# Kernel tuning notes

Hardware: AMD Instinct MI355X
Metric: run time of the kernel (lower is better)

Reference implementation:

```python
import jax, jax.numpy as jnp
import numpy as np

N = 10000       # nodes
E = 640000      # edges
D_IN = 128
D_OUT = 128
EPS = 1e-5      # LayerNorm eps (torch default)


def setup_inputs() -> dict:
    key = jax.random.key(0)
    k_x, k_e, k_w, k_b, k_g = jax.random.split(key, 5)
    x = jax.random.normal(k_x, (N, D_IN), dtype=jnp.float32)
    edge_index = jax.random.randint(k_e, (2, E), 0, N, dtype=jnp.int64)
    # GCNConv linear weight (PyG uses glorot) and bias
    lim = float(np.sqrt(6.0 / (D_IN + D_OUT)))
    W = jax.random.uniform(k_w, (D_IN, D_OUT), minval=-lim, maxval=lim, dtype=jnp.float32)
    b = jnp.zeros((D_OUT,), dtype=jnp.float32)
    # LayerNorm affine params
    gamma = jnp.ones((D_OUT,), dtype=jnp.float32)
    beta = jnp.zeros((D_OUT,), dtype=jnp.float32)
    return {"x": x, "edge_index": edge_index, "W": W, "b": b, "gamma": gamma, "beta": beta}


def reference(x, edge_index, W, b, gamma, beta):
    # --- GCNConv: A_hat = D^{-1/2} (A + I) D^{-1/2}; out = A_hat X W + b ---
    self_idx = jnp.arange(N, dtype=edge_index.dtype)
    src = jnp.concatenate([edge_index[0], self_idx])  # [E+N]
    dst = jnp.concatenate([edge_index[1], self_idx])  # [E+N]
    deg = jax.ops.segment_sum(jnp.ones_like(src, dtype=x.dtype), dst, num_segments=N)
    dinv = jnp.where(deg > 0, jax.lax.rsqrt(deg), 0.0)  # [N]
    norm = dinv[src] * dinv[dst]                        # [E+N]
    h = x @ W                                           # [N, D_OUT] transform first (cheaper)
    msg = h[src] * norm[:, None]                        # [E+N, D_OUT]
    out = jax.ops.segment_sum(msg, dst, num_segments=N) + b
    # --- LayerNorm over feature dim ---
    mu = jnp.mean(out, axis=-1, keepdims=True)
    var = jnp.mean(jnp.square(out - mu), axis=-1, keepdims=True)
    out = (out - mu) * jax.lax.rsqrt(var + EPS) * gamma + beta
    # act = Identity (last_act=ReLU is truthy -> Identity branch); dropout = eval identity; residual=False
    return out
```

## Files before the change

kernel.cpp:

```cpp
#include <hip/hip_runtime.h>
#include <hip/hip_fp16.h>

#define D 128
#define LN_EPS 1e-5f


static __device__ __forceinline__ float h2f(unsigned short h) {
    return __half2float(__builtin_bit_cast(__half, h));
}
static __device__ __forceinline__ unsigned short f2h(float f) {
    return __builtin_bit_cast(unsigned short, __float2half_rn(f));
}

__global__ __launch_bounds__(1024) void hist_kernel(const int* __restrict__ dst,
                                                    int* __restrict__ ghist,
                                                    const float* __restrict__ x,
                                                    unsigned int* __restrict__ xh,
                                                    const float* __restrict__ W,
                                                    unsigned int* __restrict__ Wh,
                                                    int N, int E, int Ec, int NH, int NW,
                                                    int C) {
    extern __shared__ int hist[];
    int c = blockIdx.x;
    bool is_hist = (c < C);
    if (is_hist)
        for (int i = threadIdx.x; i < N; i += blockDim.x) hist[i] = 0;
    int gs = gridDim.x * blockDim.x;
    int tot = NH + NW;
    for (int i = blockIdx.x * blockDim.x + threadIdx.x; i < tot; i += gs) {
        if (i < NH) {
            float2 v = ((const float2*)x)[i];
            xh[i] = (unsigned int)f2h(v.x) | ((unsigned int)f2h(v.y) << 16);
        } else {
            float2 v = ((const float2*)W)[i - NH];
            Wh[i - NH] = (unsigned int)f2h(v.x) | ((unsigned int)f2h(v.y) << 16);
        }
    }
    if (!is_hist) return;
    __syncthreads();
    int lo = c * Ec, hi = min(lo + Ec, E);
    for (int i = lo + threadIdx.x; i < hi; i += blockDim.x)
        atomicAdd(&hist[dst[i]], 1);
    __syncthreads();
    for (int i = threadIdx.x; i < N; i += blockDim.x) ghist[c * N + i] = hist[i];
}

__global__ void chunkoff_kernel(int* __restrict__ ghist, int* __restrict__ deg,
                                int N, int C) {
    int n = blockIdx.x * blockDim.x + threadIdx.x;
    if (n < N) {
        int run = 0;
        #pragma unroll 4
        for (int c = 0; c < C; c++) {
            int t = ghist[c * N + n];
            ghist[c * N + n] = run;
            run += t;
        }
        deg[n] = run;
    }
}

__global__ __launch_bounds__(1024) void scan_kernel(const int* __restrict__ deg,
                                                    int* __restrict__ rowptr,
                                                    int* __restrict__ fill,
                                                    float* __restrict__ dinv, int N) {
    __shared__ int s_wsum[16];
    __shared__ int s_woff[16];
    __shared__ int s_carry;
    int t = threadIdx.x;
    int lane = t & 63, w = t >> 6;
    if (t == 0) s_carry = 0;
    __syncthreads();
    for (int base = 0; base < N; base += 1024) {
        int i = base + t;
        int v = (i < N) ? deg[i] : 0;
        int incl = v;
        #pragma unroll
        for (int off = 1; off < 64; off <<= 1) {
            int y = __shfl_up(incl, off);
            if (lane >= off) incl += y;
        }
        if (lane == 63) s_wsum[w] = incl;
        __syncthreads();
        if (t == 0) {
            int run = s_carry;
            #pragma unroll
            for (int k = 0; k < 16; k++) { s_woff[k] = run; run += s_wsum[k]; }
            s_carry = run;
        }
        __syncthreads();
        if (i < N) {
            int rp = s_woff[w] + (incl - v);
            rowptr[i] = rp;
            fill[i] = rp;
            dinv[i] = rsqrtf((float)(v + 1));
        }
    }
    if (t == 0) rowptr[N] = s_carry;
}

__global__ __launch_bounds__(1024) void scatter_kernel(const int* __restrict__ src,
                                                       const int* __restrict__ dst,
                                                       const int* __restrict__ rowptr,
                                                       const int* __restrict__ goff,
                                                       unsigned short* __restrict__ csr,
                                                       int N, int E, int Ec) {
    extern __shared__ int cnt[];
    int c = blockIdx.x;
    for (int i = threadIdx.x; i < N; i += blockDim.x)
        cnt[i] = rowptr[i] + goff[c * N + i];
    __syncthreads();
    int lo = c * Ec, hi = min(lo + Ec, E);
    for (int i = lo + threadIdx.x; i < hi; i += blockDim.x) {
        int d = dst[i];
        int pos = atomicAdd(&cnt[d], 1);
        csr[pos] = (unsigned short)src[i];
    }
}

__global__ __launch_bounds__(512) void fused_fp16(const unsigned int* __restrict__ xh,
                                                  const unsigned int* __restrict__ Wh,
                                                  const int* __restrict__ rowptr,
                                                  const unsigned short* __restrict__ csr,
                                                  const float* __restrict__ dinv,
                                                  const float* __restrict__ bias,
                                                  const float* __restrict__ gamma,
                                                  const float* __restrict__ beta,
                                                  float* __restrict__ out, int N) {
    int w = threadIdx.x >> 6, lane = threadIdx.x & 63;
    int node = blockIdx.x * 8 + w;
    if (node >= N) return;
    float dn = dinv[node];

    unsigned int xv = xh[node * 64 + lane];
    float a0 = h2f((unsigned short)xv) * dn * dn;
    float a1 = h2f((unsigned short)(xv >> 16)) * dn * dn;

    int start = rowptr[node], end = rowptr[node + 1];
    int base = start;
    for (; base + 64 <= end; base += 64) {
        int s = csr[base + lane];
        float wt = dinv[s] * dn;
        #pragma unroll 8
        for (int k = 0; k < 64; k++) {
            int sk = __shfl(s, k);
            float wk = __shfl(wt, k);
            unsigned int hv = xh[sk * 64 + lane];
            a0 += h2f((unsigned short)hv) * wk;
            a1 += h2f((unsigned short)(hv >> 16)) * wk;
        }
    }
    int rem = end - base;
    if (rem > 0) {
        int s = 0; float wt = 0.f;
        if (lane < rem) { s = csr[base + lane]; wt = dinv[s] * dn; }
        for (int k = 0; k < rem; k++) {
            int sk = __shfl(s, k);
            float wk = __shfl(wt, k);
            unsigned int hv = xh[sk * 64 + lane];
            a0 += h2f((unsigned short)hv) * wk;
            a1 += h2f((unsigned short)(hv >> 16)) * wk;
        }
    }

    int c0 = lane * 2;
    float y0 = bias[c0], y1 = bias[c0 + 1];
    #pragma unroll 8
    for (int k = 0; k < 64; k++) {
        float g0 = __shfl(a0, k);
        float g1 = __shfl(a1, k);
        unsigned int w0 = Wh[(2 * k) * 64 + lane];
        unsigned int w1 = Wh[(2 * k + 1) * 64 + lane];
        y0 += g0 * h2f((unsigned short)w0) + g1 * h2f((unsigned short)w1);
        y1 += g0 * h2f((unsigned short)(w0 >> 16)) + g1 * h2f((unsigned short)(w1 >> 16));
    }

    float sum = y0 + y1, sq = y0 * y0 + y1 * y1;
    #pragma unroll
    for (int off = 32; off > 0; off >>= 1) {
        sum += __shfl_xor(sum, off);
        sq  += __shfl_xor(sq, off);
    }
    float mean = sum * (1.0f / D);
    float var  = sq * (1.0f / D) - mean * mean;
    float inv  = rsqrtf(var + LN_EPS);
    float o0 = (y0 - mean) * inv * gamma[c0] + beta[c0];
    float o1 = (y1 - mean) * inv * gamma[c0 + 1] + beta[c0 + 1];
    *(float2*)(out + (size_t)node * D + c0) = make_float2(o0, o1);
}


__global__ void deg_kernel(const int* __restrict__ dst, int* __restrict__ deg, int E) {
    int e = blockIdx.x * blockDim.x + threadIdx.x;
    if (e < E) atomicAdd(&deg[dst[e]], 1);
}
__global__ void fill_kernel(const int* __restrict__ src, const int* __restrict__ dst,
                            int* __restrict__ fill, unsigned short* __restrict__ csr, int E) {
    int e = blockIdx.x * blockDim.x + threadIdx.x;
    if (e < E) {
        int pos = atomicAdd(&fill[dst[e]], 1);
        csr[pos] = (unsigned short)src[e];
    }
}
__global__ __launch_bounds__(512) void fused_fp32(const float* __restrict__ x,
                                                  const float* __restrict__ W,
                                                  const int* __restrict__ rowptr,
                                                  const unsigned short* __restrict__ csr,
                                                  const float* __restrict__ dinv,
                                                  const float* __restrict__ bias,
                                                  const float* __restrict__ gamma,
                                                  const float* __restrict__ beta,
                                                  float* __restrict__ out, int N) {
    __shared__ float sW[D * D];
    {
        const float4* Wv = (const float4*)W;
        float4* sWv = (float4*)sW;
        #pragma unroll
        for (int i = 0; i < (D * D / 4) / 512; i++)
            sWv[threadIdx.x + i * 512] = Wv[threadIdx.x + i * 512];
    }
    __syncthreads();
    int w = threadIdx.x >> 6, lane = threadIdx.x & 63;
    int node = blockIdx.x * 8 + w;
    if (node >= N) return;
    float dn = dinv[node];
    int c0 = lane * 2;
    float2 xv = *(const float2*)(x + (size_t)node * D + c0);
    float a0 = xv.x * dn * dn, a1 = xv.y * dn * dn;
    int start = rowptr[node], end = rowptr[node + 1];
    int base = start;
    for (; base + 64 <= end; base += 64) {
        int s = csr[base + lane];
        float wt = dinv[s] * dn;
        #pragma unroll 8
        for (int k = 0; k < 64; k++) {
            int sk = __shfl(s, k);
            float wk = __shfl(wt, k);
            float2 xs = *(const float2*)(x + (size_t)sk * D + c0);
            a0 += xs.x * wk; a1 += xs.y * wk;
        }
    }
    int rem = end - base;
    if (rem > 0) {
        int s = 0; float wt = 0.f;
        if (lane < rem) { s = csr[base + lane]; wt = dinv[s] * dn; }
        for (int k = 0; k < rem; k++) {
            int sk = __shfl(s, k);
            float wk = __shfl(wt, k);
            float2 xs = *(const float2*)(x + (size_t)sk * D + c0);
            a0 += xs.x * wk; a1 += xs.y * wk;
        }
    }
    float y0 = bias[c0], y1 = bias[c0 + 1];
    #pragma unroll 8
    for (int k = 0; k < 64; k++) {
        float g0 = __shfl(a0, k);
        float g1 = __shfl(a1, k);
        float2 w0 = *(const float2*)(sW + (2 * k) * D + c0);
        float2 w1 = *(const float2*)(sW + (2 * k + 1) * D + c0);
        y0 += g0 * w0.x + g1 * w1.x;
        y1 += g0 * w0.y + g1 * w1.y;
    }
    float sum = y0 + y1, sq = y0 * y0 + y1 * y1;
    #pragma unroll
    for (int off = 32; off > 0; off >>= 1) {
        sum += __shfl_xor(sum, off);
        sq  += __shfl_xor(sq, off);
    }
    float mean = sum * (1.0f / D);
    float var  = sq * (1.0f / D) - mean * mean;
    float inv  = rsqrtf(var + LN_EPS);
    float o0 = (y0 - mean) * inv * gamma[c0] + beta[c0];
    float o1 = (y1 - mean) * inv * gamma[c0 + 1] + beta[c0 + 1];
    *(float2*)(out + (size_t)node * D + c0) = make_float2(o0, o1);
}

extern "C" void kernel_launch(void* const* d_in, const int* in_sizes, int n_in,
                              void* d_out, int out_size, void* d_ws, size_t ws_size,
                              hipStream_t stream) {
    const float* x     = (const float*)d_in[0];
    const int*   ei    = (const int*)d_in[1];
    const float* W     = (const float*)d_in[2];
    const float* bias  = (const float*)d_in[3];
    const float* gamma = (const float*)d_in[4];
    const float* beta  = (const float*)d_in[5];
    float*       out   = (float*)d_out;

    int N = in_sizes[0] / D;
    int E = in_sizes[1] / 2;
    const int* src = ei;
    const int* dst = ei + E;

    char* ws = (char*)d_ws;
    size_t off = 0;
    auto carve = [&](size_t bytes) { size_t p = off; off = (off + bytes + 15) & ~15UL; return (void*)(ws + p); };
    int*            deg    = (int*)           carve((size_t)N * 4);
    int*            rowptr = (int*)           carve((size_t)(N + 1) * 4);
    int*            fill   = (int*)           carve((size_t)N * 4);
    float*          dinv   = (float*)         carve((size_t)N * 4);
    unsigned short* csr    = (unsigned short*)carve((size_t)E * 2);
    unsigned short* xhbuf  = (unsigned short*)carve((size_t)N * D * 2);
    unsigned int*   Wh     = (unsigned int*)  carve((size_t)D * D / 2 * 4);
    size_t fixed_end = off;

    int C = 0;
    if (ws_size > fixed_end + 16) {
        size_t avail = ws_size - fixed_end - 16;
        size_t cmax = avail / ((size_t)N * 4);
        C = (int)((cmax > 64) ? 64 : cmax);
    }

    if (C >= 8) {
        int* ghist = (int*)carve((size_t)C * N * 4);
        unsigned int* xh = (unsigned int*)xhbuf;
        int Ec = (E + C - 1) / C;
        int NH = N * (D / 2);
        int NW = D * D / 2;
        size_t lds = (size_t)N * 4;
        int hist_grid = (256 > C) ? 256 : C;
        hist_kernel<<<hist_grid, 1024, lds, stream>>>(dst, ghist, x, xh, W, Wh,
                                                      N, E, Ec, NH, NW, C);
        chunkoff_kernel<<<(N + 255) / 256, 256, 0, stream>>>(ghist, deg, N, C);
        scan_kernel<<<1, 1024, 0, stream>>>(deg, rowptr, fill, dinv, N);
        scatter_kernel<<<C, 1024, lds, stream>>>(src, dst, rowptr, ghist, csr, N, E, Ec);
        fused_fp16<<<(N + 7) / 8, 512, 0, stream>>>(xh, Wh, rowptr, csr, dinv, bias, gamma, beta, out, N);
    } else {
        hipMemsetAsync(deg, 0, (size_t)N * 4, stream);
        deg_kernel<<<(E + 255) / 256, 256, 0, stream>>>(dst, deg, E);
        scan_kernel<<<1, 1024, 0, stream>>>(deg, rowptr, fill, dinv, N);
        fill_kernel<<<(E + 255) / 256, 256, 0, stream>>>(src, dst, fill, csr, E);
        fused_fp32<<<(N + 7) / 8, 512, 0, stream>>>(x, W, rowptr, csr, dinv, bias, gamma, beta, out, N);
    }
}
```

Measured before the change: 154.4 us.

## Merge CSR build stages into one persistent kernel with grid barriers

Replaces the hist, chunk-offset, single-block scan and scatter kernels with one build kernel of C blocks that synchronise through atomic grid barriers. It also parallelises the prefix scan across blocks with a two-level blocksum scan. The aggregation kernel now has two waves share each node, splitting the edge list, and combines the results in LDS before an LDS-based matvec and LayerNorm. The aim is to cut kernel launch gaps and the serial scan. The risks are that the fp16 conversion now runs on only C blocks, and that the spin barriers rely on all C blocks being co-resident.

```diff
diff --git a/kernel.cpp b/kernel.cpp
--- a/kernel.cpp
+++ b/kernel.cpp
@@ -12,22 +12,34 @@
     return __builtin_bit_cast(unsigned short, __float2half_rn(f));
 }
 
-__global__ __launch_bounds__(1024) void hist_kernel(const int* __restrict__ dst,
-                                                    int* __restrict__ ghist,
-                                                    const float* __restrict__ x,
-                                                    unsigned int* __restrict__ xh,
-                                                    const float* __restrict__ W,
-                                                    unsigned int* __restrict__ Wh,
-                                                    int N, int E, int Ec, int NH, int NW,
-                                                    int C) {
-    extern __shared__ int hist[];
+static __device__ __forceinline__ void gbar(int* cnt, int target) {
+    __syncthreads();
+    if (threadIdx.x == 0) {
+        __hip_atomic_fetch_add(cnt, 1, __ATOMIC_RELEASE, __HIP_MEMORY_SCOPE_AGENT);
+        while (__hip_atomic_load(cnt, __ATOMIC_ACQUIRE, __HIP_MEMORY_SCOPE_AGENT) < target) {
+            __builtin_amdgcn_s_sleep(1);
+        }
+    }
+    __syncthreads();
+}
+
+__global__ __launch_bounds__(1024) void build_kernel(
+        const int* __restrict__ src, const int* __restrict__ dst,
+        const float* __restrict__ x, const float* __restrict__ W,
+        unsigned int* __restrict__ xh, unsigned int* __restrict__ Wh,
+        int* __restrict__ ghist, int* __restrict__ blocksum,
+        int* __restrict__ rowptr, float* __restrict__ dinv,
+        unsigned short* __restrict__ csr, int* __restrict__ bar,
+        int N, int E, int Ec, int NH, int NW, int C) {
+    extern __shared__ int lds[];
     int c = blockIdx.x;
-    bool is_hist = (c < C);
-    if (is_hist)
-        for (int i = threadIdx.x; i < N; i += blockDim.x) hist[i] = 0;
-    int gs = gridDim.x * blockDim.x;
+    int tid = threadIdx.x;
+    int lane = tid & 63, wv = tid >> 6;
+
+    for (int i = tid; i < N; i += 1024) lds[i] = 0;
+    int gs = gridDim.x * 1024;
     int tot = NH + NW;
-    for (int i = blockIdx.x * blockDim.x + threadIdx.x; i < tot; i += gs) {
+    for (int i = c * 1024 + tid; i < tot; i += gs) {
         if (i < NH) {
             float2 v = ((const float2*)x)[i];
             xh[i] = (unsigned int)f2h(v.x) | ((unsigned int)f2h(v.y) << 16);
@@ -36,30 +48,162 @@
             Wh[i - NH] = (unsigned int)f2h(v.x) | ((unsigned int)f2h(v.y) << 16);
         }
     }
-    if (!is_hist) return;
     __syncthreads();
     int lo = c * Ec, hi = min(lo + Ec, E);
-    for (int i = lo + threadIdx.x; i < hi; i += blockDim.x)
-        atomicAdd(&hist[dst[i]], 1);
-    __syncthreads();
-    for (int i = threadIdx.x; i < N; i += blockDim.x) ghist[c * N + i] = hist[i];
-}
-
-__global__ void chunkoff_kernel(int* __restrict__ ghist, int* __restrict__ deg,
-                                int N, int C) {
-    int n = blockIdx.x * blockDim.x + threadIdx.x;
-    if (n < N) {
+    for (int i = lo + tid; i < hi; i += 1024)
+        atomicAdd(&lds[dst[i]], 1);
+    __syncthreads();
+    for (int i = tid; i < N; i += 1024) ghist[c * N + i] = lds[i];
+    gbar(bar + 0, C);
+
+    int nper = (N + C - 1) / C;
+    int n0 = c * nper;
+    int nn = min(nper, N - n0); if (nn < 0) nn = 0;
+    int mydeg = 0;
+    if (tid < nn) {
+        int n = n0 + tid;
         int run = 0;
-        #pragma unroll 4
-        for (int c = 0; c < C; c++) {
-            int t = ghist[c * N + n];
-            ghist[c * N + n] = run;
+        #pragma unroll 8
+        for (int cc = 0; cc < C; cc++) {
+            int t = ghist[cc * N + n];
+            ghist[cc * N + n] = run;
             run += t;
         }
-        deg[n] = run;
-    }
-}
-
+        mydeg = run;
+        dinv[n] = rsqrtf((float)(run + 1));
+    }
+    int incl = mydeg;
+    #pragma unroll
+    for (int off = 1; off < 64; off <<= 1) {
+        int y = __shfl_up(incl, off);
+        if (lane >= off) incl += y;
+    }
+    __syncthreads();
+    if (lane == 63) lds[wv] = incl;
+    __syncthreads();
+    if (tid == 0) {
+        int run = 0;
+        #pragma unroll
+        for (int k = 0; k < 16; k++) { int t = lds[k]; lds[k] = run; run += t; }
+        lds[16] = run;
+    }
+    __syncthreads();
+    int excl = lds[wv] + incl - mydeg;
+    if (tid < nn) rowptr[n0 + tid] = excl;
+    if (tid == 0) blocksum[c] = lds[16];
+    gbar(bar + 1, C);
+
+    __syncthreads();
+    if (wv == 0) {
+        int bs = (lane < C) ? blocksum[lane] : 0;
+        int inc2 = bs;
+        #pragma unroll
+        for (int off = 1; off < 64; off <<= 1) {
+            int y = __shfl_up(inc2, off);
+            if (lane >= off) inc2 += y;
+        }
+        if (lane == C - 1) lds[17] = inc2;
+        if (lane == c)     lds[18] = inc2 - bs;
+    }
+    __syncthreads();
+    int base = lds[18];
+    if (tid < nn) rowptr[n0 + tid] += base;
+    if (c == C - 1 && tid == 0) rowptr[N] = lds[17];
+    gbar(bar + 2, C);
+
+    for (int i = tid; i < N; i += 1024) lds[i] = rowptr[i] + ghist[c * N + i];
+    __syncthreads();
+    for (int i = lo + tid; i < hi; i += 1024) {
+        int d = dst[i];
+        int pos = atomicAdd(&lds[d], 1);
+        csr[pos] = (unsigned short)src[i];
+    }
+}
+
+__global__ __launch_bounds__(512) void fused2(const unsigned int* __restrict__ xh,
+                                              const unsigned int* __restrict__ Wh,
+                                              const int* __restrict__ rowptr,
+                                              const unsigned short* __restrict__ csr,
+                                              const float* __restrict__ dinv,
+                                              const float* __restrict__ bias,
+                                              const float* __restrict__ gamma,
+                                              const float* __restrict__ beta,
+                                              float* __restrict__ out, int N) {
+    __shared__ float sAgg[4][D];
+    __shared__ float sRed[4][2][2];
+    int wv = threadIdx.x >> 6, lane = threadIdx.x & 63;
+    int pair = wv >> 1, half = wv & 1;
+    int node = blockIdx.x * 4 + pair;
+    bool valid = (node < N);
+    int node_c = valid ? node : (N - 1);
+    float dn = dinv[node_c];
+
+    float a0 = 0.f, a1 = 0.f;
+    if (half == 0) {
+        unsigned int xv = xh[node_c * 64 + lane];
+        a0 = h2f((unsigned short)xv) * dn * dn;
+        a1 = h2f((unsigned short)(xv >> 16)) * dn * dn;
+    }
+    int start = rowptr[node_c], end = rowptr[node_c + 1];
+    for (int bs = start + half * 64; bs < end; bs += 128) {
+        int cnt = min(64, end - bs);
+        if (cnt == 64) {
+            int s = csr[bs + lane];
+            float wt = dinv[s] * dn;
+            #pragma unroll 8
+            for (int k = 0; k < 64; k++) {
+                int sk = __shfl(s, k);
+                float wk = __shfl(wt, k);
+                unsigned int hv = xh[sk * 64 + lane];
+                a0 += h2f((unsigned short)hv) * wk;
+                a1 += h2f((unsigned short)(hv >> 16)) * wk;
+            }
+        } else {
+            int s = 0; float wt = 0.f;
+            if (lane < cnt) { s = csr[bs + lane]; wt = dinv[s] * dn; }
+            for (int k = 0; k < cnt; k++) {
+                int sk = __shfl(s, k);
+                float wk = __shfl(wt, k);
+                unsigned int hv = xh[sk * 64 + lane];
+                a0 += h2f((unsigned short)hv) * wk;
+                a1 += h2f((unsigned short)(hv >> 16)) * wk;
+            }
+        }
+    }
+    if (half == 0) { sAgg[pair][2 * lane] = a0; sAgg[pair][2 * lane + 1] = a1; }
+    __syncthreads();
+    if (half == 1) { sAgg[pair][2 * lane] += a0; sAgg[pair][2 * lane + 1] += a1; }
+    __syncthreads();
+
+    const unsigned short* Wh16 = (const unsigned short*)Wh;
+    int cc = half * 64 + lane;
+    float y = bias[cc];
+    #pragma unroll 8
+    for (int k = 0; k < D; k++)
+        y += sAgg[pair][k] * h2f(Wh16[k * D + cc]);
+
+    float sum = y, sq = y * y;
+    #pragma unroll
+    for (int off = 32; off > 0; off >>= 1) {
+        sum += __shfl_xor(sum, off);
+        sq  += __shfl_xor(sq, off);
+    }
+    if (lane == 0) { sRed[pair][half][0] = sum; sRed[pair][half][1] = sq; }
+    __syncthreads();
+    float tsum = sRed[pair][0][0] + sRed[pair][1][0];
+    float tsq  = sRed[pair][0][1] + sRed[pair][1][1];
+    float mean = tsum * (1.0f / D);
+    float var  = tsq * (1.0f / D) - mean * mean;
+    float inv  = rsqrtf(var + LN_EPS);
+    float o = (y - mean) * inv * gamma[cc] + beta[cc];
+    if (valid) out[(size_t)node * D + cc] = o;
+}
+
+
+__global__ void deg_kernel(const int* __restrict__ dst, int* __restrict__ deg, int E) {
+    int e = blockIdx.x * blockDim.x + threadIdx.x;
+    if (e < E) atomicAdd(&deg[dst[e]], 1);
+}
 __global__ __launch_bounds__(1024) void scan_kernel(const int* __restrict__ deg,
                                                     int* __restrict__ rowptr,
                                                     int* __restrict__ fill,
@@ -97,102 +241,6 @@
         }
     }
     if (t == 0) rowptr[N] = s_carry;
-}
-
-__global__ __launch_bounds__(1024) void scatter_kernel(const int* __restrict__ src,
-                                                       const int* __restrict__ dst,
-                                                       const int* __restrict__ rowptr,
-                                                       const int* __restrict__ goff,
-                                                       unsigned short* __restrict__ csr,
-                                                       int N, int E, int Ec) {
-    extern __shared__ int cnt[];
-    int c = blockIdx.x;
-    for (int i = threadIdx.x; i < N; i += blockDim.x)
-        cnt[i] = rowptr[i] + goff[c * N + i];
-    __syncthreads();
-    int lo = c * Ec, hi = min(lo + Ec, E);
-    for (int i = lo + threadIdx.x; i < hi; i += blockDim.x) {
-        int d = dst[i];
-        int pos = atomicAdd(&cnt[d], 1);
-        csr[pos] = (unsigned short)src[i];
-    }
-}
-
-__global__ __launch_bounds__(512) void fused_fp16(const unsigned int* __restrict__ xh,
-                                                  const unsigned int* __restrict__ Wh,
-                                                  const int* __restrict__ rowptr,
-                                                  const unsigned short* __restrict__ csr,
-                                                  const float* __restrict__ dinv,
-                                                  const float* __restrict__ bias,
-                                                  const float* __restrict__ gamma,
-                                                  const float* __restrict__ beta,
-                                                  float* __restrict__ out, int N) {
-    int w = threadIdx.x >> 6, lane = threadIdx.x & 63;
-    int node = blockIdx.x * 8 + w;
-    if (node >= N) return;
-    float dn = dinv[node];
-
-    unsigned int xv = xh[node * 64 + lane];
-    float a0 = h2f((unsigned short)xv) * dn * dn;
-    float a1 = h2f((unsigned short)(xv >> 16)) * dn * dn;
-
-    int start = rowptr[node], end = rowptr[node + 1];
-    int base = start;
-    for (; base + 64 <= end; base += 64) {
-        int s = csr[base + lane];
-        float wt = dinv[s] * dn;
-        #pragma unroll 8
-        for (int k = 0; k < 64; k++) {
-            int sk = __shfl(s, k);
-            float wk = __shfl(wt, k);
-            unsigned int hv = xh[sk * 64 + lane];
-            a0 += h2f((unsigned short)hv) * wk;
-            a1 += h2f((unsigned short)(hv >> 16)) * wk;
-        }
-    }
-    int rem = end - base;
-    if (rem > 0) {
-        int s = 0; float wt = 0.f;
-        if (lane < rem) { s = csr[base + lane]; wt = dinv[s] * dn; }
-        for (int k = 0; k < rem; k++) {
-            int sk = __shfl(s, k);
-            float wk = __shfl(wt, k);
-            unsigned int hv = xh[sk * 64 + lane];
-            a0 += h2f((unsigned short)hv) * wk;
-            a1 += h2f((unsigned short)(hv >> 16)) * wk;
-        }
-    }
-
-    int c0 = lane * 2;
-    float y0 = bias[c0], y1 = bias[c0 + 1];
-    #pragma unroll 8
-    for (int k = 0; k < 64; k++) {
-        float g0 = __shfl(a0, k);
-        float g1 = __shfl(a1, k);
-        unsigned int w0 = Wh[(2 * k) * 64 + lane];
-        unsigned int w1 = Wh[(2 * k + 1) * 64 + lane];
-        y0 += g0 * h2f((unsigned short)w0) + g1 * h2f((unsigned short)w1);
-        y1 += g0 * h2f((unsigned short)(w0 >> 16)) + g1 * h2f((unsigned short)(w1 >> 16));
-    }
-
-    float sum = y0 + y1, sq = y0 * y0 + y1 * y1;
-    #pragma unroll
-    for (int off = 32; off > 0; off >>= 1) {
-        sum += __shfl_xor(sum, off);
-        sq  += __shfl_xor(sq, off);
-    }
-    float mean = sum * (1.0f / D);
-    float var  = sq * (1.0f / D) - mean * mean;
-    float inv  = rsqrtf(var + LN_EPS);
-    float o0 = (y0 - mean) * inv * gamma[c0] + beta[c0];
-    float o1 = (y1 - mean) * inv * gamma[c0 + 1] + beta[c0 + 1];
-    *(float2*)(out + (size_t)node * D + c0) = make_float2(o0, o1);
-}
-
-
-__global__ void deg_kernel(const int* __restrict__ dst, int* __restrict__ deg, int E) {
-    int e = blockIdx.x * blockDim.x + threadIdx.x;
-    if (e < E) atomicAdd(&deg[dst[e]], 1);
 }
 __global__ void fill_kernel(const int* __restrict__ src, const int* __restrict__ dst,
                             int* __restrict__ fill, unsigned short* __restrict__ csr, int E) {
@@ -294,13 +342,13 @@
     char* ws = (char*)d_ws;
     size_t off = 0;
     auto carve = [&](size_t bytes) { size_t p = off; off = (off + bytes + 15) & ~15UL; return (void*)(ws + p); };
-    int*            deg    = (int*)           carve((size_t)N * 4);
-    int*            rowptr = (int*)           carve((size_t)(N + 1) * 4);
-    int*            fill   = (int*)           carve((size_t)N * 4);
-    float*          dinv   = (float*)         carve((size_t)N * 4);
-    unsigned short* csr    = (unsigned short*)carve((size_t)E * 2);
-    unsigned short* xhbuf  = (unsigned short*)carve((size_t)N * D * 2);
-    unsigned int*   Wh     = (unsigned int*)  carve((size_t)D * D / 2 * 4);
+    int*            bar      = (int*)           carve(64);
+    int*            blocksum = (int*)           carve(64 * 4);
+    int*            rowptr   = (int*)           carve((size_t)(N + 1) * 4);
+    float*          dinv     = (float*)         carve((size_t)N * 4);
+    unsigned short* csr      = (unsigned short*)carve((size_t)E * 2);
+    unsigned int*   xh       = (unsigned int*)  carve((size_t)N * (D / 2) * 4);
+    unsigned int*   Wh       = (unsigned int*)  carve((size_t)D * (D / 2) * 4);
     size_t fixed_end = off;
 
     int C = 0;
@@ -310,25 +358,26 @@
         C = (int)((cmax > 64) ? 64 : cmax);
     }
 
-    if (C >= 8) {
+    if (C >= 16) {
         int* ghist = (int*)carve((size_t)C * N * 4);
-        unsigned int* xh = (unsigned int*)xhbuf;
         int Ec = (E + C - 1) / C;
         int NH = N * (D / 2);
-        int NW = D * D / 2;
+        int NW = D * (D / 2);
         size_t lds = (size_t)N * 4;
-        int hist_grid = (256 > C) ? 256 : C;
-        hist_kernel<<<hist_grid, 1024, lds, stream>>>(dst, ghist, x, xh, W, Wh,
-                                                      N, E, Ec, NH, NW, C);
-        chunkoff_kernel<<<(N + 255) / 256, 256, 0, stream>>>(ghist, deg, N, C);
-        scan_kernel<<<1, 1024, 0, stream>>>(deg, rowptr, fill, dinv, N);
-        scatter_kernel<<<C, 1024, lds, stream>>>(src, dst, rowptr, ghist, csr, N, E, Ec);
-        fused_fp16<<<(N + 7) / 8, 512, 0, stream>>>(xh, Wh, rowptr, csr, dinv, bias, gamma, beta, out, N);
+        hipMemsetAsync(bar, 0, 64, stream);
+        build_kernel<<<C, 1024, lds, stream>>>(src, dst, x, W, xh, Wh, ghist,
+                                               blocksum, rowptr, dinv, csr, bar,
+                                               N, E, Ec, NH, NW, C);
+        fused2<<<(N + 3) / 4, 512, 0, stream>>>(xh, Wh, rowptr, csr, dinv,
+                                                bias, gamma, beta, out, N);
     } else {
+        int* deg  = (int*)carve((size_t)N * 4);
+        int* fill = (int*)carve((size_t)N * 4);
         hipMemsetAsync(deg, 0, (size_t)N * 4, stream);
         deg_kernel<<<(E + 255) / 256, 256, 0, stream>>>(dst, deg, E);
         scan_kernel<<<1, 1024, 0, stream>>>(deg, rowptr, fill, dinv, N);
         fill_kernel<<<(E + 255) / 256, 256, 0, stream>>>(src, dst, fill, csr, E);
-        fused_fp32<<<(N + 7) / 8, 512, 0, stream>>>(x, W, rowptr, csr, dinv, bias, gamma, beta, out, N);
-    }
-}
+        fused_fp32<<<(N + 7) / 8, 512, 0, stream>>>(x, W, rowptr, csr, dinv,
+                                                    bias, gamma, beta, out, N);
+    }
+}
```

Result: slower. 166.3 us (+7.8%).
